# Optimization experiments

Hardware: AMD Instinct MI355X
Metric: run time of the kernel (lower is better)

Reference implementation:

```python
import jax, jax.numpy as jnp
import numpy as np

B, N, C = 16, 1024, 1024
H = 16            # num_attention_heads
D = C // H        # attention_head_size = 64

def setup_inputs() -> dict:
    key = jax.random.key(0)
    k1, k2, k3 = jax.random.split(key, 3)
    scale = 1.0 / np.sqrt(C)
    return {
        "hidden_states": jax.random.normal(k1, (B, N, C), dtype=jnp.float32),
        "qkv_w": jax.random.normal(k2, (C, 3 * C), dtype=jnp.float32) * scale,
        "qkv_b": jnp.zeros((3 * C,), dtype=jnp.float32),
        "proj_w": jax.random.normal(k3, (C, C), dtype=jnp.float32) * scale,
        "proj_b": jnp.zeros((C,), dtype=jnp.float32),
    }

def reference(hidden_states, qkv_w, qkv_b, proj_w, proj_b):
    # fused QKV projection: [B, N, 3C]
    qkv = hidden_states @ qkv_w + qkv_b
    # reshape to [3, B, H, N, D]
    qkv = qkv.reshape(B, N, 3, H, D).transpose(2, 0, 3, 1, 4)
    q, k, v = qkv[0], qkv[1], qkv[2]
    # attention scores [B, H, N, N]
    scores = jnp.einsum("bhnd,bhmd->bhnm", q, k) / jnp.sqrt(jnp.float32(D))
    probs = jax.nn.softmax(scores, axis=-1)  # dropout_p=0 -> identity
    ctx = jnp.einsum("bhnm,bhmd->bhnd", probs, v)
    ctx = ctx.transpose(0, 2, 1, 3).reshape(B, N, C)
    # output projection
    return ctx @ proj_w + proj_b
```

## Files before the change

kernel.cpp:

```cpp
#include <hip/hip_runtime.h>


#define BB 16
#define NN 1024
#define CC 1024
#define HH 16
#define DD 64
#define BN (BB * NN)
#define HEADELEMS (256 * 1024 * 64)

typedef float  f4     __attribute__((ext_vector_type(4)));
typedef __bf16 bf16x8 __attribute__((ext_vector_type(8)));
typedef __bf16 bf16x4 __attribute__((ext_vector_type(4)));
typedef short  s8v    __attribute__((ext_vector_type(8)));
typedef short  s4v    __attribute__((ext_vector_type(4)));
typedef short  s2v    __attribute__((ext_vector_type(2)));

#if __has_builtin(__builtin_amdgcn_exp2f)
#define EXP2(x) __builtin_amdgcn_exp2f(x)
#else
#define EXP2(x) exp2f(x)
#endif

__device__ __forceinline__ short f2bf(float x) {
  union { float f; unsigned u; } a; a.f = x;
  unsigned r = a.u + 0x7fffu + ((a.u >> 16) & 1u);
  return (short)(r >> 16);
}

__device__ __forceinline__ void gl_lds16(const void* g, void* l) {
  __builtin_amdgcn_global_load_lds((__attribute__((address_space(1))) void*)g,
                                   (__attribute__((address_space(3))) void*)l,
                                   16, 0, 0);
}

__device__ __forceinline__ f4 mfma16(bf16x8 a, bf16x8 b, f4 c) {
  return __builtin_amdgcn_mfma_f32_16x16x32_bf16(a, b, c, 0, 0, 0);
}

__global__ void cast_bf16(const float* __restrict__ x, short* __restrict__ y) {
  int i = (blockIdx.x * 256 + threadIdx.x) * 4;
  float4 v = *(const float4*)&x[i];
  s4v o;
  o[0] = f2bf(v.x); o[1] = f2bf(v.y); o[2] = f2bf(v.z); o[3] = f2bf(v.w);
  *(s4v*)&y[i] = o;
}

__global__ void transpose_cast(const float* __restrict__ W, short* __restrict__ Wt,
                               int K, int Nw) {
  __shared__ float tile[32][33];
  int bx = blockIdx.x, by = blockIdx.y;
  int t = threadIdx.x;
  int tc = t & 31, tr = t >> 5;
#pragma unroll
  for (int i = 0; i < 4; ++i) {
    int r = tr + i * 8;
    tile[r][tc] = W[(size_t)(by * 32 + r) * Nw + bx * 32 + tc];
  }
  __syncthreads();
#pragma unroll
  for (int i = 0; i < 4; ++i) {
    int r = tr + i * 8;
    Wt[(size_t)(bx * 32 + r) * K + by * 32 + tc] = f2bf(tile[tc][r]);
  }
}

#define GSTAGE(buf, kb)                                                        \
  {                                                                            \
    _Pragma("unroll")                                                          \
    for (int rblk = 0; rblk < 4; ++rblk) {                                     \
      int rbase = (w * 4 + rblk) * 8;                                          \
      gl_lds16(A + (size_t)(row0 + rbase + sr8) * K + (kb) + sc8 * 8,          \
               &la[buf][rbase * 64]);                                          \
      gl_lds16(Bt + (size_t)(col0 + rbase + sr8) * K + (kb) + sc8 * 8,         \
               &lb[buf][rbase * 64]);                                          \
    }                                                                          \
  }

template <int EPI>
__global__ __launch_bounds__(256, 2)
void gemm_bt(const short* __restrict__ A, const short* __restrict__ Bt,
             const float* __restrict__ bias, float* __restrict__ Cf,
             short* __restrict__ Cq, int M, int N, int K) {
  __shared__ short la[2][128 * 64];
  __shared__ short lb[2][128 * 64];
  const int t = threadIdx.x, lane = t & 63, w = t >> 6;
  int bid = blockIdx.y * gridDim.x + blockIdx.x;
  int xcd = bid & 7, sub = bid >> 3;
  int xg = sub >> 7, rem = sub & 127;
  int xb = xg * 8 + (rem & 7), yb = xcd * 16 + (rem >> 3);
  const int row0 = yb * 128, col0 = xb * 128;
  const int wm = (w & 1) * 64, wn = (w >> 1) * 64;
  const int q = lane >> 4, ln = lane & 15;
  const int sr8 = lane >> 3;
  const int sc8 = (lane & 7) ^ sr8;
  f4 acc[4][4] = {};

  GSTAGE(0, 0);
  __syncthreads();
  int cur = 0;
  for (int kb = 0; kb < K; kb += 64, cur ^= 1) {
    if (kb + 64 < K) GSTAGE(cur ^ 1, kb + 64);
#pragma unroll
    for (int ks2 = 0; ks2 < 2; ++ks2) {
      const int c8 = ks2 * 4 + q;
      const int swz = (c8 ^ (ln & 7)) * 8;
      bf16x8 af[4], bfr[4];
#pragma unroll
      for (int i = 0; i < 4; ++i) {
        af[i]  = *(const bf16x8*)&la[cur][(wm + i * 16 + ln) * 64 + swz];
        bfr[i] = *(const bf16x8*)&lb[cur][(wn + i * 16 + ln) * 64 + swz];
      }
#pragma unroll
      for (int i = 0; i < 4; ++i)
#pragma unroll
        for (int j = 0; j < 4; ++j)
          acc[i][j] = mfma16(af[i], bfr[j], acc[i][j]);
    }
    __syncthreads();
  }

#pragma unroll
  for (int i = 0; i < 4; ++i) {
    int rbase = row0 + wm + i * 16 + q * 4;
#pragma unroll
    for (int j = 0; j < 4; ++j) {
      int col = col0 + wn + j * 16 + ln;
      float bv = bias[col];
      if (EPI == 0) {
#pragma unroll
        for (int r2 = 0; r2 < 4; ++r2)
          Cf[(size_t)(rbase + r2) * N + col] = acc[i][j][r2] + bv;
      } else {
        int which = col >> 10, c = col & 1023;
        int h = c >> 6, d = c & 63;
        if (which == 2) {
          int bh = (rbase >> 10) * HH + h;
          s4v vv;
#pragma unroll
          for (int r2 = 0; r2 < 4; ++r2) vv[r2] = f2bf(acc[i][j][r2] + bv);
          *(s4v*)&Cq[(size_t)2 * HEADELEMS + ((size_t)bh * DD + d) * NN + (rbase & 1023)] = vv;
        } else {
          float scale = (which == 0) ? 0.1803368801f : 1.0f;
#pragma unroll
          for (int r2 = 0; r2 < 4; ++r2) {
            int row = rbase + r2;
            int bh = (row >> 10) * HH + h;
            size_t idx = ((size_t)bh * NN + (row & 1023)) * DD + d;
            Cq[(size_t)which * HEADELEMS + idx] = f2bf((acc[i][j][r2] + bv) * scale);
          }
        }
      }
    }
  }
}

__global__ __launch_bounds__(512, 4)
void attn(const short* __restrict__ Qg, const short* __restrict__ Kg,
          const short* __restrict__ Vtg, short* __restrict__ ctx) {
  __shared__ short sQP[256 * 64];
  __shared__ short sK[2][64 * 64];
  __shared__ short sV[2][64 * 64];
  const int t = threadIdx.x, lane = t & 63, w = t >> 6;
  const int bh = blockIdx.x, qb = blockIdx.y;
  const short* Qh = Qg + (size_t)bh * (NN * DD) + qb * 256 * DD;
  const short* Kh = Kg + (size_t)bh * (NN * DD);
  const short* Vh = Vtg + (size_t)bh * (NN * DD);

#pragma unroll
  for (int k = 0; k < 4; ++k) {
    int i = t + k * 512;
    int r = i >> 3, c = i & 7;
    gl_lds16(Qh + r * DD + ((c ^ (r & 7)) * 8), &sQP[i * 8]);
  }
  const int sr = t >> 3, sc = t & 7;
  const int ssc = ((sc ^ (sr & 7)) * 8);
  gl_lds16(Kh + sr * DD + ssc, &sK[0][t * 8]);
  gl_lds16(Vh + (size_t)sr * NN + ssc, &sV[0][t * 8]);

  __syncthreads();

  const int q = lane >> 4, ln = lane & 15;
  const int wq = w * 32;
  const int sw = ln & 7;

  bf16x8 qf[2][2];
#pragma unroll
  for (int ks = 0; ks < 2; ++ks)
#pragma unroll
    for (int g = 0; g < 2; ++g)
      qf[ks][g] = *(const bf16x8*)&sQP[(wq + g * 16 + ln) * 64 + (((ks * 4 + q) ^ sw) * 8)];

  f4 o[2][4] = {};
  float lsum0 = 0.f, lsum1 = 0.f;

  for (int kt = 0; kt < 16; ++kt) {
    const int cur = kt & 1;
    if (kt < 15) {
      const int nb = cur ^ 1;
      gl_lds16(Kh + (kt + 1) * 64 * DD + sr * DD + ssc, &sK[nb][t * 8]);
      gl_lds16(Vh + (size_t)sr * NN + (kt + 1) * 64 + ssc, &sV[nb][t * 8]);
    }

    f4 s[4][2] = {};
    __builtin_amdgcn_s_setprio(1);
#pragma unroll
    for (int ks = 0; ks < 2; ++ks)
#pragma unroll
      for (int ki = 0; ki < 4; ++ki) {
        bf16x8 kf = *(const bf16x8*)&sK[cur][(ki * 16 + ln) * 64 + (((ks * 4 + q) ^ sw) * 8)];
        s[ki][0] = mfma16(kf, qf[ks][0], s[ki][0]);
        s[ki][1] = mfma16(kf, qf[ks][1], s[ki][1]);
      }
    __builtin_amdgcn_s_setprio(0);

#pragma unroll
    for (int g = 0; g < 2; ++g)
#pragma unroll
      for (int ki = 0; ki < 4; ++ki) {
        f4 sv = s[ki][g];
        float p0 = EXP2(sv[0]), p1 = EXP2(sv[1]);
        float p2 = EXP2(sv[2]), p3 = EXP2(sv[3]);
        if (g == 0) lsum0 += (p0 + p1) + (p2 + p3);
        else        lsum1 += (p0 + p1) + (p2 + p3);
        bf16x4 pk;
        pk[0] = (__bf16)p0; pk[1] = (__bf16)p1;
        pk[2] = (__bf16)p2; pk[3] = (__bf16)p3;
        *(bf16x4*)&sQP[(wq + g * 16 + ln) * 64 +
                       (((2 * ki + (q >> 1)) ^ sw) * 8) + (q & 1) * 4] = pk;
      }

    __builtin_amdgcn_s_setprio(1);
#pragma unroll
    for (int ks = 0; ks < 2; ++ks) {
      bf16x8 vf[4];
#pragma unroll
      for (int j = 0; j < 4; ++j)
        vf[j] = *(const bf16x8*)&sV[cur][(j * 16 + ln) * 64 + (((ks * 4 + q) ^ sw) * 8)];
#pragma unroll
      for (int g = 0; g < 2; ++g) {
        bf16x8 pf = *(const bf16x8*)&sQP[(wq + g * 16 + ln) * 64 + (((ks * 4 + q) ^ sw) * 8)];
#pragma unroll
        for (int j = 0; j < 4; ++j)
          o[g][j] = mfma16(pf, vf[j], o[g][j]);
      }
    }
    __builtin_amdgcn_s_setprio(0);

    __syncthreads();
  }

#pragma unroll
  for (int g = 0; g < 2; ++g) {
    float lfull = (g == 0) ? lsum0 : lsum1;
    lfull += __shfl_xor(lfull, 16);
    lfull += __shfl_xor(lfull, 32);
#pragma unroll
    for (int r = 0; r < 4; ++r) {
      float lr = __shfl(lfull, q * 4 + r);
      float inv = 1.0f / lr;
      int token_row = qb * 256 + wq + g * 16 + q * 4 + r;
      size_t base = ((size_t)(bh >> 4) * NN + token_row) * CC + (bh & 15) * DD;
#pragma unroll
      for (int j = 0; j < 4; ++j)
        ctx[base + j * 16 + ln] = f2bf(o[g][j][r] * inv);
    }
  }
}

extern "C" void kernel_launch(void* const* d_in, const int* in_sizes, int n_in,
                              void* d_out, int out_size, void* d_ws, size_t ws_size,
                              hipStream_t stream) {
  const float* hs     = (const float*)d_in[0];
  const float* qkv_w  = (const float*)d_in[1];
  const float* qkv_b  = (const float*)d_in[2];
  const float* proj_w = (const float*)d_in[3];
  const float* proj_b = (const float*)d_in[4];

  short* ws = (short*)d_ws;
  if (ws_size < 176160768ull) return;
  short* Xbf = ws;
  short* Wq  = ws + 16777216;
  short* Wp  = ws + 19922944;
  short* Qm  = ws + 20971520;
  short* Km  = ws + 37748736;
  short* Vt  = ws + 54525952;
  short* Ctx = ws + 71303168;

  cast_bf16<<<16384, 256, 0, stream>>>(hs, Xbf);
  transpose_cast<<<dim3(96, 32), 256, 0, stream>>>(qkv_w, Wq, 1024, 3072);
  transpose_cast<<<dim3(32, 32), 256, 0, stream>>>(proj_w, Wp, 1024, 1024);

  gemm_bt<1><<<dim3(24, 128), 256, 0, stream>>>(Xbf, Wq, qkv_b, nullptr, Qm,
                                                BN, 3 * CC, CC);
  attn<<<dim3(256, 4), 512, 0, stream>>>(Qm, Km, Vt, Ctx);
  gemm_bt<0><<<dim3(8, 128), 256, 0, stream>>>(Ctx, Wp, proj_b, (float*)d_out, nullptr,
                                               BN, CC, CC);
}
```

Baseline: 393.6 us.

## Enlarge GEMM tile to 256x128 with 512 threads and triple-buffered A pipeline

The bf16 GEMM kernel moves from 128x128 tiles with 256 threads to 256x128 tiles with 512 threads (8 waves). A is now triple-buffered and prefetched two k-steps ahead, while B stays double-buffered. Full __syncthreads calls are replaced with explicit vmcnt waits plus raw s_barrier, and MFMA blocks are wrapped in setprio. The aim is more reuse of each B tile and better overlap of global-to-LDS loads with compute. The cost is higher LDS use (about 128KB) and one block per CU, which lowers occupancy, and hand-counted vmcnt waits that can silently go wrong.

```diff
diff --git a/kernel.cpp b/kernel.cpp
--- a/kernel.cpp
+++ b/kernel.cpp
@@ -65,42 +65,62 @@
   }
 }
 
-#define GSTAGE(buf, kb)                                                        \
+#define GSTAGE_A(buf, kb)                                                      \
   {                                                                            \
     _Pragma("unroll")                                                          \
     for (int rblk = 0; rblk < 4; ++rblk) {                                     \
       int rbase = (w * 4 + rblk) * 8;                                          \
       gl_lds16(A + (size_t)(row0 + rbase + sr8) * K + (kb) + sc8 * 8,          \
                &la[buf][rbase * 64]);                                          \
+    }                                                                          \
+  }
+#define GSTAGE_B(buf, kb)                                                      \
+  {                                                                            \
+    _Pragma("unroll")                                                          \
+    for (int bblk = 0; bblk < 2; ++bblk) {                                     \
+      int rbase = (w * 2 + bblk) * 8;                                          \
       gl_lds16(Bt + (size_t)(col0 + rbase + sr8) * K + (kb) + sc8 * 8,         \
                &lb[buf][rbase * 64]);                                          \
     }                                                                          \
   }
 
 template <int EPI>
-__global__ __launch_bounds__(256, 2)
+__global__ __launch_bounds__(512, 1)
 void gemm_bt(const short* __restrict__ A, const short* __restrict__ Bt,
              const float* __restrict__ bias, float* __restrict__ Cf,
              short* __restrict__ Cq, int M, int N, int K) {
-  __shared__ short la[2][128 * 64];
+  __shared__ short la[3][256 * 64];
   __shared__ short lb[2][128 * 64];
   const int t = threadIdx.x, lane = t & 63, w = t >> 6;
   int bid = blockIdx.y * gridDim.x + blockIdx.x;
   int xcd = bid & 7, sub = bid >> 3;
-  int xg = sub >> 7, rem = sub & 127;
-  int xb = xg * 8 + (rem & 7), yb = xcd * 16 + (rem >> 3);
-  const int row0 = yb * 128, col0 = xb * 128;
-  const int wm = (w & 1) * 64, wn = (w >> 1) * 64;
+  int grp = sub >> 5, rem = sub & 31;
+  int xb = grp * 4 + (rem & 3), yb = xcd * 8 + (rem >> 2);
+  const int row0 = yb * 256, col0 = xb * 128;
+  const int wm = (w >> 1) * 64, wn = (w & 1) * 64;
   const int q = lane >> 4, ln = lane & 15;
   const int sr8 = lane >> 3;
   const int sc8 = (lane & 7) ^ sr8;
   f4 acc[4][4] = {};
 
-  GSTAGE(0, 0);
-  __syncthreads();
-  int cur = 0;
-  for (int kb = 0; kb < K; kb += 64, cur ^= 1) {
-    if (kb + 64 < K) GSTAGE(cur ^ 1, kb + 64);
+  const int NT = K >> 6;
+  GSTAGE_A(0, 0);
+  GSTAGE_B(0, 0);
+  __builtin_amdgcn_sched_barrier(0);
+  GSTAGE_A(1, 64);
+  asm volatile("s_waitcnt vmcnt(4)" ::: "memory");
+  __builtin_amdgcn_s_barrier();
+  __builtin_amdgcn_sched_barrier(0);
+
+  int curA = 0;
+  for (int tt = 0; tt < NT; ++tt) {
+    if (tt + 1 < NT) GSTAGE_B((tt + 1) & 1, (tt + 1) * 64);
+    __builtin_amdgcn_sched_barrier(0);
+    if (tt + 2 < NT) {
+      int a2 = curA + 2; if (a2 >= 3) a2 -= 3;
+      GSTAGE_A(a2, (tt + 2) * 64);
+    }
+    __builtin_amdgcn_sched_barrier(0);
 #pragma unroll
     for (int ks2 = 0; ks2 < 2; ++ks2) {
       const int c8 = ks2 * 4 + q;
@@ -108,16 +128,22 @@
       bf16x8 af[4], bfr[4];
 #pragma unroll
       for (int i = 0; i < 4; ++i) {
-        af[i]  = *(const bf16x8*)&la[cur][(wm + i * 16 + ln) * 64 + swz];
-        bfr[i] = *(const bf16x8*)&lb[cur][(wn + i * 16 + ln) * 64 + swz];
-      }
+        af[i]  = *(const bf16x8*)&la[curA][(wm + i * 16 + ln) * 64 + swz];
+        bfr[i] = *(const bf16x8*)&lb[tt & 1][(wn + i * 16 + ln) * 64 + swz];
+      }
+      __builtin_amdgcn_s_setprio(1);
 #pragma unroll
       for (int i = 0; i < 4; ++i)
 #pragma unroll
         for (int j = 0; j < 4; ++j)
           acc[i][j] = mfma16(af[i], bfr[j], acc[i][j]);
-    }
-    __syncthreads();
+      __builtin_amdgcn_s_setprio(0);
+    }
+    if (tt + 2 < NT) asm volatile("s_waitcnt vmcnt(4)" ::: "memory");
+    else             asm volatile("s_waitcnt vmcnt(0)" ::: "memory");
+    __builtin_amdgcn_s_barrier();
+    __builtin_amdgcn_sched_barrier(0);
+    curA = (curA == 2) ? 0 : curA + 1;
   }
 
 #pragma unroll
@@ -291,9 +317,9 @@
   transpose_cast<<<dim3(96, 32), 256, 0, stream>>>(qkv_w, Wq, 1024, 3072);
   transpose_cast<<<dim3(32, 32), 256, 0, stream>>>(proj_w, Wp, 1024, 1024);
 
-  gemm_bt<1><<<dim3(24, 128), 256, 0, stream>>>(Xbf, Wq, qkv_b, nullptr, Qm,
-                                                BN, 3 * CC, CC);
+  gemm_bt<1><<<dim3(24, 64), 512, 0, stream>>>(Xbf, Wq, qkv_b, nullptr, Qm,
+                                               BN, 3 * CC, CC);
   attn<<<dim3(256, 4), 512, 0, stream>>>(Qm, Km, Vt, Ctx);
-  gemm_bt<0><<<dim3(8, 128), 256, 0, stream>>>(Ctx, Wp, proj_b, (float*)d_out, nullptr,
-                                               BN, CC, CC);
-}
+  gemm_bt<0><<<dim3(8, 64), 512, 0, stream>>>(Ctx, Wp, proj_b, (float*)d_out, nullptr,
+                                              BN, CC, CC);
+}
```

New measurement: 409.0 us. +3.9%, slower.

## Halve GEMM K-tile for higher occupancy and compute softmax row sums via MFMA

Applied to the files above, without the earlier changes.

The GEMM's K-step drops from 64 to 32, halving LDS per block so four blocks can fit per CU (launch bounds 256,4). The swizzle and staging layout are rewritten for 32-wide rows, and the MFMA loop gets s_setprio raised. In the attention kernel, the per-lane scalar softmax denominator accumulation and cross-lane shuffles are replaced by an extra MFMA against a vector of ones, using the same bf16-rounded probabilities as the PV product. This costs more loop iterations and barriers in the GEMM and extra MFMA work in attention, in exchange for fewer VALU and shuffle operations.

```diff
diff --git a/kernel.cpp b/kernel.cpp
--- a/kernel.cpp
+++ b/kernel.cpp
@@ -68,22 +68,22 @@
 #define GSTAGE(buf, kb)                                                        \
   {                                                                            \
     _Pragma("unroll")                                                          \
-    for (int rblk = 0; rblk < 4; ++rblk) {                                     \
-      int rbase = (w * 4 + rblk) * 8;                                          \
-      gl_lds16(A + (size_t)(row0 + rbase + sr8) * K + (kb) + sc8 * 8,          \
-               &la[buf][rbase * 64]);                                          \
-      gl_lds16(Bt + (size_t)(col0 + rbase + sr8) * K + (kb) + sc8 * 8,         \
-               &lb[buf][rbase * 64]);                                          \
+    for (int rblk = 0; rblk < 2; ++rblk) {                                     \
+      int rbase = (w * 2 + rblk) * 16;                                         \
+      gl_lds16(A + (size_t)(row0 + rbase + sr4) * K + (kb) + sc4 * 8,          \
+               &la[buf][rbase * 32]);                                          \
+      gl_lds16(Bt + (size_t)(col0 + rbase + sr4) * K + (kb) + sc4 * 8,         \
+               &lb[buf][rbase * 32]);                                          \
     }                                                                          \
   }
 
 template <int EPI>
-__global__ __launch_bounds__(256, 2)
+__global__ __launch_bounds__(256, 4)
 void gemm_bt(const short* __restrict__ A, const short* __restrict__ Bt,
              const float* __restrict__ bias, float* __restrict__ Cf,
              short* __restrict__ Cq, int M, int N, int K) {
-  __shared__ short la[2][128 * 64];
-  __shared__ short lb[2][128 * 64];
+  __shared__ short la[2][128 * 32];
+  __shared__ short lb[2][128 * 32];
   const int t = threadIdx.x, lane = t & 63, w = t >> 6;
   int bid = blockIdx.y * gridDim.x + blockIdx.x;
   int xcd = bid & 7, sub = bid >> 3;
@@ -92,31 +92,29 @@
   const int row0 = yb * 128, col0 = xb * 128;
   const int wm = (w & 1) * 64, wn = (w >> 1) * 64;
   const int q = lane >> 4, ln = lane & 15;
-  const int sr8 = lane >> 3;
-  const int sc8 = (lane & 7) ^ sr8;
+  const int sr4 = lane >> 2;
+  const int sc4 = (lane & 3) ^ (sr4 & 3);
   f4 acc[4][4] = {};
 
   GSTAGE(0, 0);
   __syncthreads();
   int cur = 0;
-  for (int kb = 0; kb < K; kb += 64, cur ^= 1) {
-    if (kb + 64 < K) GSTAGE(cur ^ 1, kb + 64);
-#pragma unroll
-    for (int ks2 = 0; ks2 < 2; ++ks2) {
-      const int c8 = ks2 * 4 + q;
-      const int swz = (c8 ^ (ln & 7)) * 8;
-      bf16x8 af[4], bfr[4];
-#pragma unroll
-      for (int i = 0; i < 4; ++i) {
-        af[i]  = *(const bf16x8*)&la[cur][(wm + i * 16 + ln) * 64 + swz];
-        bfr[i] = *(const bf16x8*)&lb[cur][(wn + i * 16 + ln) * 64 + swz];
-      }
-#pragma unroll
-      for (int i = 0; i < 4; ++i)
-#pragma unroll
-        for (int j = 0; j < 4; ++j)
-          acc[i][j] = mfma16(af[i], bfr[j], acc[i][j]);
-    }
+  for (int kb = 0; kb < K; kb += 32, cur ^= 1) {
+    if (kb + 32 < K) GSTAGE(cur ^ 1, kb + 32);
+    const int swz = (q ^ (ln & 3)) * 8;
+    bf16x8 af[4], bfr[4];
+#pragma unroll
+    for (int i = 0; i < 4; ++i) {
+      af[i]  = *(const bf16x8*)&la[cur][(wm + i * 16 + ln) * 32 + swz];
+      bfr[i] = *(const bf16x8*)&lb[cur][(wn + i * 16 + ln) * 32 + swz];
+    }
+    __builtin_amdgcn_s_setprio(1);
+#pragma unroll
+    for (int i = 0; i < 4; ++i)
+#pragma unroll
+      for (int j = 0; j < 4; ++j)
+        acc[i][j] = mfma16(af[i], bfr[j], acc[i][j]);
+    __builtin_amdgcn_s_setprio(0);
     __syncthreads();
   }
 
@@ -191,8 +189,12 @@
     for (int g = 0; g < 2; ++g)
       qf[ks][g] = *(const bf16x8*)&sQP[(wq + g * 16 + ln) * 64 + (((ks * 4 + q) ^ sw) * 8)];
 
+  bf16x8 onesb;
+#pragma unroll
+  for (int j = 0; j < 8; ++j) onesb[j] = (__bf16)1.0f;
+
   f4 o[2][4] = {};
-  float lsum0 = 0.f, lsum1 = 0.f;
+  f4 l4[2] = {};
 
   for (int kt = 0; kt < 16; ++kt) {
     const int cur = kt & 1;
@@ -219,13 +221,9 @@
 #pragma unroll
       for (int ki = 0; ki < 4; ++ki) {
         f4 sv = s[ki][g];
-        float p0 = EXP2(sv[0]), p1 = EXP2(sv[1]);
-        float p2 = EXP2(sv[2]), p3 = EXP2(sv[3]);
-        if (g == 0) lsum0 += (p0 + p1) + (p2 + p3);
-        else        lsum1 += (p0 + p1) + (p2 + p3);
         bf16x4 pk;
-        pk[0] = (__bf16)p0; pk[1] = (__bf16)p1;
-        pk[2] = (__bf16)p2; pk[3] = (__bf16)p3;
+        pk[0] = (__bf16)EXP2(sv[0]); pk[1] = (__bf16)EXP2(sv[1]);
+        pk[2] = (__bf16)EXP2(sv[2]); pk[3] = (__bf16)EXP2(sv[3]);
         *(bf16x4*)&sQP[(wq + g * 16 + ln) * 64 +
                        (((2 * ki + (q >> 1)) ^ sw) * 8) + (q & 1) * 4] = pk;
       }
@@ -240,6 +238,7 @@
 #pragma unroll
       for (int g = 0; g < 2; ++g) {
         bf16x8 pf = *(const bf16x8*)&sQP[(wq + g * 16 + ln) * 64 + (((ks * 4 + q) ^ sw) * 8)];
+        l4[g] = mfma16(pf, onesb, l4[g]);
 #pragma unroll
         for (int j = 0; j < 4; ++j)
           o[g][j] = mfma16(pf, vf[j], o[g][j]);
@@ -251,21 +250,16 @@
   }
 
 #pragma unroll
-  for (int g = 0; g < 2; ++g) {
-    float lfull = (g == 0) ? lsum0 : lsum1;
-    lfull += __shfl_xor(lfull, 16);
-    lfull += __shfl_xor(lfull, 32);
+  for (int g = 0; g < 2; ++g)
 #pragma unroll
     for (int r = 0; r < 4; ++r) {
-      float lr = __shfl(lfull, q * 4 + r);
-      float inv = 1.0f / lr;
+      float inv = 1.0f / l4[g][r];
       int token_row = qb * 256 + wq + g * 16 + q * 4 + r;
       size_t base = ((size_t)(bh >> 4) * NN + token_row) * CC + (bh & 15) * DD;
 #pragma unroll
       for (int j = 0; j < 4; ++j)
         ctx[base + j * 16 + ln] = f2bf(o[g][j][r] * inv);
     }
-  }
 }
 
 extern "C" void kernel_launch(void* const* d_in, const int* in_sizes, int n_in,
```

Result: faster. 380.7 us (-3.3%).
